# Performance work log

Measured on AMD Instinct MI355X. Metric: run time of the kernel, lower is better.

The kernel has to match this reference:

```python
import jax, jax.numpy as jnp
import numpy as np

EMBED = 1024
HEADS = 16
HEAD_DIM = EMBED // HEADS


def setup_inputs() -> dict:
    key = jax.random.key(0)
    k1, k2, k3, k4, k5 = jax.random.split(key, 5)
    B, S, E = 4, 2048, EMBED
    scale = 1.0 / np.sqrt(E)
    return {
        "tensor": jax.random.normal(k1, (B, S, E), dtype=jnp.float32),
        "in_proj_w": jax.random.normal(k2, (3 * E, E), dtype=jnp.float32) * scale,
        "in_proj_b": jax.random.normal(k3, (3 * E,), dtype=jnp.float32) * 0.02,
        "out_proj_w": jax.random.normal(k4, (E, E), dtype=jnp.float32) * scale,
        "out_proj_b": jax.random.normal(k5, (E,), dtype=jnp.float32) * 0.02,
        "causal_mask": 1,
    }


def reference(tensor, in_proj_w, in_proj_b, out_proj_w, out_proj_b, causal_mask):
    B, S, E = tensor.shape
    H, D = HEADS, HEAD_DIM
    # fused qkv projection (torch Linear: x @ W.T + b)
    qkv = tensor @ in_proj_w.T + in_proj_b  # [B, S, 3E]
    q, k, v = jnp.split(qkv, 3, axis=-1)
    # [B, S, E] -> [B, H, S, D]
    q = q.reshape(B, S, H, D).transpose(0, 2, 1, 3)
    k = k.reshape(B, S, H, D).transpose(0, 2, 1, 3)
    v = v.reshape(B, S, H, D).transpose(0, 2, 1, 3)
    scores = jnp.einsum("bhqd,bhkd->bhqk", q, k)  # [B, H, S, S]
    if causal_mask:
        mask = jnp.triu(jnp.ones((S, S), dtype=bool), k=1)
        scores = jnp.where(mask, -jnp.inf, scores)
    scores = scores / np.sqrt(D).astype(np.float32)
    attn = jax.nn.softmax(scores, axis=-1)
    out = jnp.einsum("bhqk,bhkd->bhqd", attn, v)  # [B, H, S, D]
    out = out.transpose(0, 2, 1, 3).reshape(B, S, E)
    return out @ out_proj_w.T + out_proj_b
```

## Files before the change

### kernel.cpp

```cpp
#include <hip/hip_runtime.h>
#include <hip/hip_bf16.h>

#define B_  4
#define S_  2048
#define E_  1024
#define H_  16
#define D_  64
#define M_  (B_*S_)
#define N3_ (3*E_)

typedef __bf16 bf16;
typedef bf16  bf16x4 __attribute__((ext_vector_type(4)));
typedef bf16  bf16x8 __attribute__((ext_vector_type(8)));
typedef float f32x4  __attribute__((ext_vector_type(4)));

#define SC2 0.18033688011112043f

__device__ __forceinline__ f32x4 mfma16(bf16x8 a, bf16x8 b, f32x4 c) {
    return __builtin_amdgcn_mfma_f32_16x16x32_bf16(a, b, c, 0, 0, 0);
}

typedef const __attribute__((address_space(1))) void* gas_t;
typedef __attribute__((address_space(3))) void* las_t;
__device__ __forceinline__ void gl_lds16(const void* g, void* l) {
    __builtin_amdgcn_global_load_lds((gas_t)g, (las_t)l, 16, 0, 0);
}

#define WAITCNT_VM4() __builtin_amdgcn_s_waitcnt(0x0F74)
#define WAITCNT_VM0() __builtin_amdgcn_s_waitcnt(0x0F70)

__global__ __launch_bounds__(256) void cvt_all(const float* __restrict__ x,
                                               const float* __restrict__ w_in,
                                               const float* __restrict__ w_out,
                                               bf16* __restrict__ Xbf,
                                               bf16* __restrict__ Wqkv,
                                               bf16* __restrict__ Wo) {
    const int n1 = M_ * E_ / 4, n2 = N3_ * E_ / 4, n3 = E_ * E_ / 4;
    int i = blockIdx.x * blockDim.x + threadIdx.x;
    const float* src; bf16* dst; int j;
    if (i < n1)           { src = x;     dst = Xbf;  j = i; }
    else if (i < n1 + n2) { src = w_in;  dst = Wqkv; j = i - n1; }
    else if (i < n1 + n2 + n3) { src = w_out; dst = Wo; j = i - n1 - n2; }
    else return;
    float4 v = *(const float4*)(src + (size_t)j * 4);
    bf16x4 o;
    o[0] = (bf16)v.x; o[1] = (bf16)v.y; o[2] = (bf16)v.z; o[3] = (bf16)v.w;
    *(bf16x4*)(dst + (size_t)j * 4) = o;
}

__global__ __launch_bounds__(256) void gemm_qkv(const bf16* __restrict__ X,
                                                const bf16* __restrict__ W,
                                                const float* __restrict__ bias,
                                                bf16* __restrict__ QKV,
                                                bf16* __restrict__ Vt) {
    __shared__ __align__(16) bf16 As[128 * 64];
    __shared__ __align__(16) bf16 Bs[128 * 64];
    const int t = threadIdx.x;
    const int wav = t >> 6, lane = t & 63, quad = lane >> 4, l15 = lane & 15;
    const int m0 = blockIdx.y * 128, n0 = blockIdx.x * 128;
    const int wr = (wav >> 1) * 64, wc = (wav & 1) * 64;
    const int srow = t >> 3;
    const int swz  = ((t & 7) ^ (srow & 7)) * 8;
    const bool isV = (n0 >= 2 * E_);

    const bf16* Ablk = X + (size_t)m0 * E_;
    const bf16* Bblk = W + (size_t)n0 * E_;
    f32x4 acc[4][4] = {};

    for (int kk = 0; kk < E_; kk += 64) {
        __syncthreads();
        #pragma unroll
        for (int ps = 0; ps < 4; ++ps) {
            gl_lds16(Ablk + (size_t)(srow + ps * 32) * E_ + kk + swz, As + (size_t)(t + ps * 256) * 8);
            gl_lds16(Bblk + (size_t)(srow + ps * 32) * E_ + kk + swz, Bs + (size_t)(t + ps * 256) * 8);
        }
        __syncthreads();
        #pragma unroll
        for (int ks = 0; ks < 2; ++ks) {
            bf16x8 af[4], bw[4];
            #pragma unroll
            for (int i = 0; i < 4; ++i) {
                const int ra = wr + i * 16 + l15;
                const int rb = wc + i * 16 + l15;
                const int cx = ((ks * 4 + quad) ^ (l15 & 7)) * 8;
                af[i] = *(const bf16x8*)&As[ra * 64 + cx];
                bw[i] = *(const bf16x8*)&Bs[rb * 64 + cx];
            }
            if (!isV) {
                #pragma unroll
                for (int i = 0; i < 4; ++i)
                    #pragma unroll
                    for (int j = 0; j < 4; ++j)
                        acc[i][j] = mfma16(af[i], bw[j], acc[i][j]);
            } else {
                #pragma unroll
                for (int i = 0; i < 4; ++i)
                    #pragma unroll
                    for (int j = 0; j < 4; ++j)
                        acc[i][j] = mfma16(bw[i], af[j], acc[i][j]);
            }
        }
    }
    if (!isV) {
        #pragma unroll
        for (int i = 0; i < 4; ++i)
            #pragma unroll
            for (int j = 0; j < 4; ++j)
                #pragma unroll
                for (int r = 0; r < 4; ++r) {
                    int mg = m0 + wr + i * 16 + quad * 4 + r;
                    int ng = n0 + wc + j * 16 + l15;
                    float v = acc[i][j][r] + bias[ng];
                    int which = ng >> 10, rem = ng & 1023;
                    if (which == 0) v *= SC2;
                    int h = rem >> 6, d = rem & 63;
                    int b = mg >> 11, s = mg & 2047;
                    QKV[(size_t)which * (B_ * H_ * S_ * D_) +
                        (((size_t)(b * H_ + h) * S_ + s) * D_ + d)] = (bf16)v;
                }
    } else {
        #pragma unroll
        for (int i = 0; i < 4; ++i)
            #pragma unroll
            for (int j = 0; j < 4; ++j)
                #pragma unroll
                for (int r = 0; r < 4; ++r) {
                    int ng = n0 + wc + i * 16 + quad * 4 + r;
                    int mg = m0 + wr + j * 16 + l15;
                    float v = acc[i][j][r] + bias[ng];
                    int rem = ng & 1023;
                    int h = rem >> 6, d = rem & 63;
                    int b = mg >> 11, s = mg & 2047;
                    Vt[(((size_t)(b * H_ + h) * D_ + d) * S_) + s] = (bf16)v;
                }
    }
}

__global__ __launch_bounds__(512, 4) void attn8(const bf16* __restrict__ Q,
                                                const bf16* __restrict__ K,
                                                const bf16* __restrict__ Vt,
                                                bf16* __restrict__ O) {
    __shared__ __align__(16) bf16 Ks[2][128 * 64];
    __shared__ __align__(16) bf16 Vs[2][64 * 128];
    __shared__ __align__(16) bf16 Ps[8][16 * 64];

    const int t = threadIdx.x;
    const int wav = t >> 6, lane = t & 63, quad = lane >> 4, l15 = lane & 15;
    const int p  = blockIdx.x >> 6;
    const int bh = blockIdx.x & 63;

    const bf16* Qb = Q  + (size_t)bh * S_ * D_;
    const bf16* Kb = K  + (size_t)bh * S_ * D_;
    const bf16* Vb = Vt + (size_t)bh * (size_t)D_ * S_;

    const int kr0 = t >> 3;
    const int kswz = ((t & 7) ^ (kr0 & 7)) * 8;
    const int vr0 = t >> 4;
    const int vc  = t & 15;
    const int vkey = ((vc >> 3) * 64) + (((vc & 7) ^ (vr0 & 7)) * 8);

    bf16* Pw = &Ps[wav][0];
    const int pswz = l15 & 7;

    const int b = bh >> 4, h = bh & 15;

    #pragma unroll 1
    for (int phase = 0; phase < 2; ++phase) {
        const int qb  = phase ? (15 - p) : p;
        const int q0w = qb * 128 + wav * 16;
        const int qg  = q0w + l15;
        const int niter = qb + 1;

        __builtin_amdgcn_s_barrier();
        gl_lds16(Kb + (size_t)kr0 * D_ + kswz,        &Ks[0][(size_t)t * 8]);
        gl_lds16(Kb + (size_t)(kr0 + 64) * D_ + kswz, &Ks[0][(size_t)(t + 512) * 8]);
        gl_lds16(Vb + (size_t)vr0 * S_ + vkey,        &Vs[0][(size_t)t * 8]);
        gl_lds16(Vb + (size_t)(vr0 + 32) * S_ + vkey, &Vs[0][(size_t)(t + 512) * 8]);

        bf16x8 qf0 = *(const bf16x8*)&Qb[(size_t)(q0w + l15) * D_ + quad * 8];
        bf16x8 qf1 = *(const bf16x8*)&Qb[(size_t)(q0w + l15) * D_ + 32 + quad * 8];

        f32x4 oacc[4] = {};
        f32x4 psum = {0.f, 0.f, 0.f, 0.f};

        #pragma unroll 1
        for (int it = 0; it < niter; ++it) {
            const int key0 = it * 128;
            const int cur = it & 1;
            const bf16* Kc = &Ks[cur][0];
            const bf16* Vc = &Vs[cur][0];

            __builtin_amdgcn_s_barrier();
            if (it + 1 < niter) {
                const int kn = key0 + 128;
                bf16* Kd = &Ks[1 - cur][0];
                bf16* Vd = &Vs[1 - cur][0];
                gl_lds16(Kb + (size_t)(kn + kr0) * D_ + kswz,        &Kd[(size_t)t * 8]);
                gl_lds16(Kb + (size_t)(kn + kr0 + 64) * D_ + kswz,   &Kd[(size_t)(t + 512) * 8]);
                gl_lds16(Vb + (size_t)vr0 * S_ + kn + vkey,          &Vd[(size_t)t * 8]);
                gl_lds16(Vb + (size_t)(vr0 + 32) * S_ + kn + vkey,   &Vd[(size_t)(t + 512) * 8]);
                WAITCNT_VM4();
            } else {
                WAITCNT_VM0();
            }
            __builtin_amdgcn_s_barrier();

            #pragma unroll
            for (int hh = 0; hh < 2; ++hh) {
                const int key0h = key0 + hh * 64;
                if (key0h > q0w + 15) continue;

                f32x4 sacc[4];
                #pragma unroll
                for (int mt = 0; mt < 4; ++mt) {
                    const int krow = hh * 64 + mt * 16 + l15;
                    bf16x8 kf0 = *(const bf16x8*)&Kc[krow * 64 + ((quad ^ pswz) * 8)];
                    bf16x8 kf1 = *(const bf16x8*)&Kc[krow * 64 + (((4 + quad) ^ pswz) * 8)];
                    f32x4 a = {};
                    a = mfma16(kf0, qf0, a);
                    a = mfma16(kf1, qf1, a);
                    sacc[mt] = a;
                }

                #pragma unroll
                for (int mt = 0; mt < 4; ++mt) {
                    if (key0h + mt * 16 + 15 > q0w) {
                        #pragma unroll
                        for (int r = 0; r < 4; ++r) {
                            int key = key0h + mt * 16 + quad * 4 + r;
                            sacc[mt][r] = (key > qg) ? -3e38f : sacc[mt][r];
                        }
                    }
                }

                #pragma unroll
                for (int mt = 0; mt < 4; ++mt) {
                    bf16x4 pk;
                    #pragma unroll
                    for (int r = 0; r < 4; ++r) {
                        float pv = __builtin_amdgcn_exp2f(sacc[mt][r]);
                        psum[r] += pv;
                        pk[r] = (bf16)pv;
                    }
                    const int pc = ((mt * 2 + (quad >> 1)) ^ pswz) * 8 + (quad & 1) * 4;
                    *(bf16x4*)&Pw[l15 * 64 + pc] = pk;
                }

                bf16x8 pf0 = *(const bf16x8*)&Pw[l15 * 64 + ((quad ^ pswz) * 8)];
                bf16x8 pf1 = *(const bf16x8*)&Pw[l15 * 64 + (((4 + quad) ^ pswz) * 8)];
                #pragma unroll
                for (int nt = 0; nt < 4; ++nt) {
                    const int vrow = nt * 16 + l15;
                    bf16x8 vf0 = *(const bf16x8*)&Vc[vrow * 128 + ((hh * 8 + (quad ^ pswz)) * 8)];
                    bf16x8 vf1 = *(const bf16x8*)&Vc[vrow * 128 + ((hh * 8 + ((4 + quad) ^ pswz)) * 8)];
                    oacc[nt] = mfma16(pf0, vf0, oacc[nt]);
                    oacc[nt] = mfma16(pf1, vf1, oacc[nt]);
                }
            }
        }

        float rsum = psum[0] + psum[1] + psum[2] + psum[3];
        rsum += __shfl_xor(rsum, 16);
        rsum += __shfl_xor(rsum, 32);
        const float linv = 1.0f / rsum;

        #pragma unroll
        for (int rr = 0; rr < 4; ++rr) {
            float li = __shfl(linv, quad * 4 + rr);
            const int q = q0w + quad * 4 + rr;
            #pragma unroll
            for (int nt = 0; nt < 4; ++nt)
                O[((size_t)b * S_ + q) * E_ + h * D_ + nt * 16 + l15] =
                    (bf16)(oacc[nt][rr] * li);
        }
    }
}

#define STG_A(dst, kk, ps) gl_lds16(Ablk + (size_t)(srow + (ps)*64)*E_ + (kk) + swz, (dst) + (size_t)(t + (ps)*512)*8)
#define STG_B(dst, kk, ps) gl_lds16(Bblk + (size_t)(srow + (ps)*64)*E_ + (kk) + swz, (dst) + (size_t)(t + (ps)*512)*8)
#define LDF(base, row, ks) (*(const bf16x8*)&(base)[(row)*64 + ((((ks)*4 + quad) ^ ((row)&7))*8)])

__global__ __launch_bounds__(512, 2) void gemm_out(const bf16* __restrict__ A,
                                                   const bf16* __restrict__ W,
                                                   const float* __restrict__ bias,
                                                   float* __restrict__ out) {
    __shared__ __align__(16) bf16 As[3][256 * 64];
    __shared__ __align__(16) bf16 Bs[3][128 * 64];
    const int t = threadIdx.x;
    const int wav = t >> 6, lane = t & 63, quad = lane >> 4, l15 = lane & 15;
    const int m0 = blockIdx.y * 256, n0 = blockIdx.x * 128;
    const int wro = (wav >> 1) * 64, wco = (wav & 1) * 64;
    const int srow = t >> 3;
    const int swz  = ((t & 7) ^ (srow & 7)) * 8;

    const bf16* Ablk = A + (size_t)m0 * E_;
    const bf16* Bblk = W + (size_t)n0 * E_;
    f32x4 acc[4][4] = {};

    {
        bf16 *Ac = &As[0][0], *An = &As[1][0], *Af = &As[2][0];
        bf16 *Bc = &Bs[0][0], *Bn = &Bs[1][0], *Bf = &Bs[2][0];
        STG_A(Ac, 0, 0);  STG_A(Ac, 0, 1);  STG_A(Ac, 0, 2);  STG_A(Ac, 0, 3);
        STG_B(Bc, 0, 0);  STG_B(Bc, 0, 1);
        STG_A(An, 64, 0); STG_A(An, 64, 1); STG_A(An, 64, 2); STG_A(An, 64, 3);
        STG_B(Bn, 64, 0); STG_B(Bn, 64, 1);
        for (int kt = 0; kt < 16; ++kt) {
            if (kt < 15) asm volatile("s_waitcnt vmcnt(6)\n\ts_barrier" ::: "memory");
            else         asm volatile("s_waitcnt vmcnt(0)\n\ts_barrier" ::: "memory");
            const int kk2 = (kt + 2) * 64;
            const bool st = (kt < 14);
            bf16x8 af[2][2], bw[4][2];
            #pragma unroll
            for (int i2 = 0; i2 < 2; ++i2) {
                int ra = wro + i2 * 16 + l15;
                af[i2][0] = LDF(Ac, ra, 0); af[i2][1] = LDF(Ac, ra, 1);
            }
            #pragma unroll
            for (int j = 0; j < 4; ++j) {
                int rb = wco + j * 16 + l15;
                bw[j][0] = LDF(Bc, rb, 0); bw[j][1] = LDF(Bc, rb, 1);
            }
            if (st) { STG_A(Af, kk2, 0); STG_A(Af, kk2, 1); STG_B(Bf, kk2, 0); }
            __builtin_amdgcn_s_setprio(1);
            #pragma unroll
            for (int i2 = 0; i2 < 2; ++i2)
                #pragma unroll
                for (int j = 0; j < 4; ++j) {
                    acc[i2][j] = mfma16(af[i2][0], bw[j][0], acc[i2][j]);
                    acc[i2][j] = mfma16(af[i2][1], bw[j][1], acc[i2][j]);
                }
            __builtin_amdgcn_s_setprio(0);
            asm volatile("s_barrier" ::: "memory");
            #pragma unroll
            for (int i2 = 0; i2 < 2; ++i2) {
                int ra = wro + (2 + i2) * 16 + l15;
                af[i2][0] = LDF(Ac, ra, 0); af[i2][1] = LDF(Ac, ra, 1);
            }
            if (st) { STG_A(Af, kk2, 2); STG_A(Af, kk2, 3); STG_B(Bf, kk2, 1); }
            __builtin_amdgcn_s_setprio(1);
            #pragma unroll
            for (int i2 = 0; i2 < 2; ++i2)
                #pragma unroll
                for (int j = 0; j < 4; ++j) {
                    acc[2 + i2][j] = mfma16(af[i2][0], bw[j][0], acc[2 + i2][j]);
                    acc[2 + i2][j] = mfma16(af[i2][1], bw[j][1], acc[2 + i2][j]);
                }
            __builtin_amdgcn_s_setprio(0);
            bf16* tp;
            tp = Ac; Ac = An; An = Af; Af = tp;
            tp = Bc; Bc = Bn; Bn = Bf; Bf = tp;
        }
    }

    #pragma unroll
    for (int i = 0; i < 4; ++i)
        #pragma unroll
        for (int j = 0; j < 4; ++j)
            #pragma unroll
            for (int r = 0; r < 4; ++r) {
                int mg = m0 + wro + i * 16 + quad * 4 + r;
                int ng = n0 + wco + j * 16 + l15;
                out[(size_t)mg * E_ + ng] = acc[i][j][r] + bias[ng];
            }
}

extern "C" void kernel_launch(void* const* d_in, const int* in_sizes, int n_in,
                              void* d_out, int out_size, void* d_ws, size_t ws_size,
                              hipStream_t stream) {
    const float* x     = (const float*)d_in[0];
    const float* w_in  = (const float*)d_in[1];
    const float* b_in  = (const float*)d_in[2];
    const float* w_out = (const float*)d_in[3];
    const float* b_out = (const float*)d_in[4];
    float* out = (float*)d_out;

    char* ws = (char*)d_ws;
    bf16* Xbf  = (bf16*)ws; ws += (size_t)M_ * E_ * 2;
    bf16* Wqkv = (bf16*)ws; ws += (size_t)N3_ * E_ * 2;
    bf16* Wo   = (bf16*)ws; ws += (size_t)E_ * E_ * 2;
    bf16* QKV  = (bf16*)ws; ws += (size_t)2 * B_ * H_ * S_ * D_ * 2;
    bf16* Vt   = (bf16*)ws; ws += (size_t)B_ * H_ * S_ * D_ * 2;
    bf16* Obf  = Xbf;

    const int nCvt = (M_ * E_ + N3_ * E_ + E_ * E_) / 4;
    cvt_all<<<(nCvt + 255) / 256, 256, 0, stream>>>(x, w_in, w_out, Xbf, Wqkv, Wo);

    gemm_qkv<<<dim3(N3_ / 128, M_ / 128), 256, 0, stream>>>(Xbf, Wqkv, b_in, QKV, Vt);

    bf16* Qp = QKV;
    bf16* Kp = QKV + (size_t)B_ * H_ * S_ * D_;

    attn8<<<dim3(8 * B_ * H_), 512, 0, stream>>>(Qp, Kp, Vt, Obf);

    gemm_out<<<dim3(E_ / 128, M_ / 256), 512, 0, stream>>>(Obf, Wo, b_out, out);
}
```

Measured before the change: 232.2 us.

## Triple-buffer 64-key K/V tiles in attention and raise priority around MFMA

```diff
diff --git a/kernel.cpp b/kernel.cpp
--- a/kernel.cpp
+++ b/kernel.cpp
@@ -27,6 +27,7 @@
 }
 
 #define WAITCNT_VM4() __builtin_amdgcn_s_waitcnt(0x0F74)
+#define WAITCNT_VM2() __builtin_amdgcn_s_waitcnt(0x0F72)
 #define WAITCNT_VM0() __builtin_amdgcn_s_waitcnt(0x0F70)
 
 __global__ __launch_bounds__(256) void cvt_all(const float* __restrict__ x,
@@ -140,8 +141,8 @@
                                                 const bf16* __restrict__ K,
                                                 const bf16* __restrict__ Vt,
                                                 bf16* __restrict__ O) {
-    __shared__ __align__(16) bf16 Ks[2][128 * 64];
-    __shared__ __align__(16) bf16 Vs[2][64 * 128];
+    __shared__ __align__(16) bf16 Ks[3][64 * 64];
+    __shared__ __align__(16) bf16 Vs[3][64 * 64];
     __shared__ __align__(16) bf16 Ps[8][16 * 64];
 
     const int t = threadIdx.x;
@@ -153,12 +154,8 @@
     const bf16* Kb = K  + (size_t)bh * S_ * D_;
     const bf16* Vb = Vt + (size_t)bh * (size_t)D_ * S_;
 
-    const int kr0 = t >> 3;
-    const int kswz = ((t & 7) ^ (kr0 & 7)) * 8;
-    const int vr0 = t >> 4;
-    const int vc  = t & 15;
-    const int vkey = ((vc >> 3) * 64) + (((vc & 7) ^ (vr0 & 7)) * 8);
-
+    const int srow = t >> 3;
+    const int swz  = ((t & 7) ^ (srow & 7)) * 8;
     bf16* Pw = &Ps[wav][0];
     const int pswz = l15 & 7;
 
@@ -169,13 +166,13 @@
         const int qb  = phase ? (15 - p) : p;
         const int q0w = qb * 128 + wav * 16;
         const int qg  = q0w + l15;
-        const int niter = qb + 1;
+        const int niter = 2 * qb + 2;
 
         __builtin_amdgcn_s_barrier();
-        gl_lds16(Kb + (size_t)kr0 * D_ + kswz,        &Ks[0][(size_t)t * 8]);
-        gl_lds16(Kb + (size_t)(kr0 + 64) * D_ + kswz, &Ks[0][(size_t)(t + 512) * 8]);
-        gl_lds16(Vb + (size_t)vr0 * S_ + vkey,        &Vs[0][(size_t)t * 8]);
-        gl_lds16(Vb + (size_t)(vr0 + 32) * S_ + vkey, &Vs[0][(size_t)(t + 512) * 8]);
+        gl_lds16(Kb + (size_t)srow * D_ + swz,        &Ks[0][(size_t)t * 8]);
+        gl_lds16(Vb + (size_t)srow * S_ + swz,        &Vs[0][(size_t)t * 8]);
+        gl_lds16(Kb + (size_t)(64 + srow) * D_ + swz, &Ks[1][(size_t)t * 8]);
+        gl_lds16(Vb + (size_t)srow * S_ + 64 + swz,   &Vs[1][(size_t)t * 8]);
 
         bf16x8 qf0 = *(const bf16x8*)&Qb[(size_t)(q0w + l15) * D_ + quad * 8];
         bf16x8 qf1 = *(const bf16x8*)&Qb[(size_t)(q0w + l15) * D_ + 32 + quad * 8];
@@ -185,78 +182,79 @@
 
         #pragma unroll 1
         for (int it = 0; it < niter; ++it) {
-            const int key0 = it * 128;
-            const int cur = it & 1;
+            const int key0 = it * 64;
+            const int cur = it % 3;
             const bf16* Kc = &Ks[cur][0];
             const bf16* Vc = &Vs[cur][0];
 
             __builtin_amdgcn_s_barrier();
-            if (it + 1 < niter) {
+            if (it + 2 < niter) {
                 const int kn = key0 + 128;
-                bf16* Kd = &Ks[1 - cur][0];
-                bf16* Vd = &Vs[1 - cur][0];
-                gl_lds16(Kb + (size_t)(kn + kr0) * D_ + kswz,        &Kd[(size_t)t * 8]);
-                gl_lds16(Kb + (size_t)(kn + kr0 + 64) * D_ + kswz,   &Kd[(size_t)(t + 512) * 8]);
-                gl_lds16(Vb + (size_t)vr0 * S_ + kn + vkey,          &Vd[(size_t)t * 8]);
-                gl_lds16(Vb + (size_t)(vr0 + 32) * S_ + kn + vkey,   &Vd[(size_t)(t + 512) * 8]);
+                const int nb = (it + 2) % 3;
+                gl_lds16(Kb + (size_t)(kn + srow) * D_ + swz, &Ks[nb][(size_t)t * 8]);
+                gl_lds16(Vb + (size_t)srow * S_ + kn + swz,   &Vs[nb][(size_t)t * 8]);
                 WAITCNT_VM4();
+            } else if (it + 1 < niter) {
+                WAITCNT_VM2();
             } else {
                 WAITCNT_VM0();
             }
             __builtin_amdgcn_s_barrier();
 
-            #pragma unroll
-            for (int hh = 0; hh < 2; ++hh) {
-                const int key0h = key0 + hh * 64;
-                if (key0h > q0w + 15) continue;
-
-                f32x4 sacc[4];
-                #pragma unroll
-                for (int mt = 0; mt < 4; ++mt) {
-                    const int krow = hh * 64 + mt * 16 + l15;
-                    bf16x8 kf0 = *(const bf16x8*)&Kc[krow * 64 + ((quad ^ pswz) * 8)];
-                    bf16x8 kf1 = *(const bf16x8*)&Kc[krow * 64 + (((4 + quad) ^ pswz) * 8)];
-                    f32x4 a = {};
-                    a = mfma16(kf0, qf0, a);
-                    a = mfma16(kf1, qf1, a);
-                    sacc[mt] = a;
-                }
-
-                #pragma unroll
-                for (int mt = 0; mt < 4; ++mt) {
-                    if (key0h + mt * 16 + 15 > q0w) {
-                        #pragma unroll
-                        for (int r = 0; r < 4; ++r) {
-                            int key = key0h + mt * 16 + quad * 4 + r;
-                            sacc[mt][r] = (key > qg) ? -3e38f : sacc[mt][r];
-                        }
-                    }
-                }
-
-                #pragma unroll
-                for (int mt = 0; mt < 4; ++mt) {
-                    bf16x4 pk;
+            if (key0 > q0w + 15) continue;
+
+            f32x4 sacc[4];
+            __builtin_amdgcn_s_setprio(1);
+            #pragma unroll
+            for (int mt = 0; mt < 4; ++mt) {
+                const int krow = mt * 16 + l15;
+                const int sw = krow & 7;
+                bf16x8 kf0 = *(const bf16x8*)&Kc[krow * 64 + ((quad ^ sw) * 8)];
+                bf16x8 kf1 = *(const bf16x8*)&Kc[krow * 64 + (((4 + quad) ^ sw) * 8)];
+                f32x4 a = {};
+                a = mfma16(kf0, qf0, a);
+                a = mfma16(kf1, qf1, a);
+                sacc[mt] = a;
+            }
+            __builtin_amdgcn_s_setprio(0);
+
+            #pragma unroll
+            for (int mt = 0; mt < 4; ++mt) {
+                if (key0 + mt * 16 + 15 > q0w) {
                     #pragma unroll
                     for (int r = 0; r < 4; ++r) {
-                        float pv = __builtin_amdgcn_exp2f(sacc[mt][r]);
-                        psum[r] += pv;
-                        pk[r] = (bf16)pv;
+                        int key = key0 + mt * 16 + quad * 4 + r;
+                        sacc[mt][r] = (key > qg) ? -3e38f : sacc[mt][r];
                     }
-                    const int pc = ((mt * 2 + (quad >> 1)) ^ pswz) * 8 + (quad & 1) * 4;
-                    *(bf16x4*)&Pw[l15 * 64 + pc] = pk;
-                }
-
-                bf16x8 pf0 = *(const bf16x8*)&Pw[l15 * 64 + ((quad ^ pswz) * 8)];
-                bf16x8 pf1 = *(const bf16x8*)&Pw[l15 * 64 + (((4 + quad) ^ pswz) * 8)];
-                #pragma unroll
-                for (int nt = 0; nt < 4; ++nt) {
-                    const int vrow = nt * 16 + l15;
-                    bf16x8 vf0 = *(const bf16x8*)&Vc[vrow * 128 + ((hh * 8 + (quad ^ pswz)) * 8)];
-                    bf16x8 vf1 = *(const bf16x8*)&Vc[vrow * 128 + ((hh * 8 + ((4 + quad) ^ pswz)) * 8)];
-                    oacc[nt] = mfma16(pf0, vf0, oacc[nt]);
-                    oacc[nt] = mfma16(pf1, vf1, oacc[nt]);
-                }
-            }
+                }
+            }
+
+            #pragma unroll
+            for (int mt = 0; mt < 4; ++mt) {
+                bf16x4 pk;
+                #pragma unroll
+                for (int r = 0; r < 4; ++r) {
+                    float pv = __builtin_amdgcn_exp2f(sacc[mt][r]);
+                    psum[r] += pv;
+                    pk[r] = (bf16)pv;
+                }
+                const int pc = ((mt * 2 + (quad >> 1)) ^ pswz) * 8 + (quad & 1) * 4;
+                *(bf16x4*)&Pw[l15 * 64 + pc] = pk;
+            }
+
+            bf16x8 pf0 = *(const bf16x8*)&Pw[l15 * 64 + ((quad ^ pswz) * 8)];
+            bf16x8 pf1 = *(const bf16x8*)&Pw[l15 * 64 + (((4 + quad) ^ pswz) * 8)];
+            __builtin_amdgcn_s_setprio(1);
+            #pragma unroll
+            for (int nt = 0; nt < 4; ++nt) {
+                const int vrow = nt * 16 + l15;
+                const int sw = vrow & 7;
+                bf16x8 vf0 = *(const bf16x8*)&Vc[vrow * 64 + ((quad ^ sw) * 8)];
+                bf16x8 vf1 = *(const bf16x8*)&Vc[vrow * 64 + (((4 + quad) ^ sw) * 8)];
+                oacc[nt] = mfma16(pf0, vf0, oacc[nt]);
+                oacc[nt] = mfma16(pf1, vf1, oacc[nt]);
+            }
+            __builtin_amdgcn_s_setprio(0);
         }
 
         float rsum = psum[0] + psum[1] + psum[2] + psum[3];
```

After: 234.8 us. No clear change (+1.1%).
